# Kernel tuning notes

Hardware: AMD Instinct MI355X
Metric: run time of the kernel (lower is better)

## Reference

```python
import jax, jax.numpy as jnp
import numpy as np

B, S, I, H, F1, C = 1024, 512, 50, 64, 32, 2


def setup_inputs() -> dict:
    key = jax.random.key(0)
    ks = jax.random.split(key, 9)
    s_ih = 1.0 / np.sqrt(H)
    return {
        "x": jax.random.normal(ks[0], (B, S, I), dtype=jnp.float32),
        # PyTorch LSTM params, gate order (i, f, g, o) stacked along dim 0
        "W_ih": jax.random.uniform(ks[1], (4 * H, I), jnp.float32, -s_ih, s_ih),
        "W_hh": jax.random.uniform(ks[2], (4 * H, H), jnp.float32, -s_ih, s_ih),
        "b_ih": jax.random.uniform(ks[3], (4 * H,), jnp.float32, -s_ih, s_ih),
        "b_hh": jax.random.uniform(ks[4], (4 * H,), jnp.float32, -s_ih, s_ih),
        "W1": jax.random.uniform(ks[5], (F1, H), jnp.float32, -s_ih, s_ih),
        "b1": jax.random.uniform(ks[6], (F1,), jnp.float32, -s_ih, s_ih),
        "W2": jax.random.uniform(ks[7], (C, F1), jnp.float32, -1.0 / np.sqrt(F1), 1.0 / np.sqrt(F1)),
        "b2": jax.random.uniform(ks[8], (C,), jnp.float32, -1.0 / np.sqrt(F1), 1.0 / np.sqrt(F1)),
    }


def _lstm_last(x, W_ih, W_hh, b_ih, b_hh):
    # Precompute input contribution for all timesteps in one big GEMM: [B,S,4H]
    xg = jnp.einsum("bsi,gi->bsg", x, W_ih) + b_ih + b_hh
    Bn = x.shape[0]
    Hn = W_hh.shape[1]
    h0 = jnp.zeros((Bn, Hn), dtype=x.dtype)
    c0 = jnp.zeros((Bn, Hn), dtype=x.dtype)

    def step(carry, xt):
        h, c = carry
        g = xt + h @ W_hh.T  # [B,4H]
        i_g, f_g, g_g, o_g = jnp.split(g, 4, axis=-1)
        i_g = jax.nn.sigmoid(i_g)
        f_g = jax.nn.sigmoid(f_g)
        g_g = jnp.tanh(g_g)
        o_g = jax.nn.sigmoid(o_g)
        c_new = f_g * c + i_g * g_g
        h_new = o_g * jnp.tanh(c_new)
        return (h_new, c_new), None

    (h_last, _), _ = jax.lax.scan(step, (h0, c0), xg.transpose(1, 0, 2))
    return h_last  # == out[:, -1, :]


def reference(x, W_ih, W_hh, b_ih, b_hh, W1, b1, W2, b2):
    last_out = _lstm_last(x, W_ih, W_hh, b_ih, b_hh)
    # Dropout is identity in eval mode (deterministic reference)
    h = jax.nn.relu(last_out @ W1.T + b1)
    return h @ W2.T + b2  # [B, num_classes]
```

## Files before the change

### kernel.cpp

```cpp
#include <hip/hip_runtime.h>
#include <math.h>


#define S_LEN  512
#define I_DIM  50
#define H_DIM  64
#define BB     4
#define TC     16
#define NCH    (S_LEN / TC)
#define KROW   40
#define XROW   72
#define XSHALF (BB * TC * XROW)
#define NXE    (BB * TC * I_DIM)
#define F1_DIM 32
#define C_DIM  2
#define ILO    (1.0f / 2048.0f)

typedef __attribute__((ext_vector_type(8))) _Float16 f16x8;
typedef __attribute__((ext_vector_type(4))) float    f32x4;

__device__ __forceinline__ float fast_rcp(float x) { return __builtin_amdgcn_rcpf(x); }
__device__ __forceinline__ float sigm(float v) { return fast_rcp(1.0f + __expf(-v)); }
__device__ __forceinline__ float tanh_fast(float v) {
    return 1.0f - 2.0f * fast_rcp(__expf(2.0f * v) + 1.0f);
}

__device__ __forceinline__ void load_wfrag(const float* __restrict__ Wih,
                                           const float* __restrict__ Whh,
                                           int ktg, int row, int hk,
                                           f16x8& bh, f16x8& bl) {
    #pragma unroll
    for (int j = 0; j < 8; ++j) {
        const int kk = ktg * 32 + hk * 8 + j;
        float wv;
        if (ktg < 2) wv = (kk < I_DIM) ? Wih[row * I_DIM + kk] : 0.0f;
        else         wv = Whh[row * H_DIM + (kk - 64)];
        const _Float16 h = (_Float16)wv;
        bh[j] = h;
        bl[j] = (_Float16)((wv - (float)h) * 2048.0f);
    }
}
__device__ __forceinline__ void load_wfrag_hi(const float* __restrict__ Whh,
                                              int ktg, int row, int hk, f16x8& bh) {
    #pragma unroll
    for (int j = 0; j < 8; ++j) {
        const int kk = ktg * 32 + hk * 8 + j;
        bh[j] = (_Float16)Whh[row * H_DIM + (kk - 64)];
    }
}

#define MFMA16(A, B, C) __builtin_amdgcn_mfma_f32_16x16x32_f16(A, B, C, 0, 0, 0)

#define BAR() do { asm volatile("s_waitcnt lgkmcnt(0)" ::: "memory"); \
                   __builtin_amdgcn_s_barrier(); } while (0)

__global__ __launch_bounds__(512, 1)
void lstm_mfma(const float* __restrict__ x,
               const float* __restrict__ W_ih, const float* __restrict__ W_hh,
               const float* __restrict__ b_ih, const float* __restrict__ b_hh,
               const float* __restrict__ W1,  const float* __restrict__ b1,
               const float* __restrict__ W2,  const float* __restrict__ b2,
               float* __restrict__ out)
{
    __shared__ __align__(16) _Float16 Hst[2][2][16][KROW];
    __shared__ __align__(16) _Float16 Xs[2][BB * TC][XROW];
    __shared__ __align__(16) float    XGb[2][TC][BB][H_DIM][4];
    __shared__ float f1buf[BB][F1_DIM];

    const int u  = threadIdx.x;
    const int w  = u >> 6;
    const int l  = u & 63;
    const int c  = l & 15;
    const int hk = l >> 4;
    const int b0 = blockIdx.x * BB;
    const bool is_scan = (w < 4);
    const int q  = w & 3;
    const f32x4 Z4 = {0.f, 0.f, 0.f, 0.f};

    f16x8 s00h, s01h, s10h, s11h, s20h, s21h, s30h, s31h;
    f16x8 g00h, g00l, g01h, g01l, g10h, g10l, g11h, g11l,
          g20h, g20l, g21h, g21l, g30h, g30l, g31h, g31l;
    float bs0 = 0.f, bs1 = 0.f, bs2 = 0.f, bs3 = 0.f;
    float cst = 0.0f;

    f16x8 ga0, ga1;
    f32x4 G0, H0, G1, H1, G2, H2, G3, H3;

    const float *xp0=x,*xp1=x,*xp2=x,*xp3=x,*xp4=x,*xp5=x,*xp6=x,
                *xp7=x,*xp8=x,*xp9=x,*xp10=x,*xp11=x,*xp12=x;
    int  ld0=0,ld1=0,ld2=0,ld3=0,ld4=0,ld5=0,ld6=0,ld7=0,ld8=0,ld9=0,ld10=0,ld11=0,ld12=0;
    bool v0=false,v1=false,v2=false,v3=false,v4=false,v5=false,v6=false,
         v7=false,v8=false,v9=false,v10=false,v11=false,v12=false;

    if (is_scan) {
        const int base = 16 * w + c;
        load_wfrag_hi(W_hh, 2, 0 * H_DIM + base, hk, s00h);
        load_wfrag_hi(W_hh, 3, 0 * H_DIM + base, hk, s01h);
        load_wfrag_hi(W_hh, 2, 1 * H_DIM + base, hk, s10h);
        load_wfrag_hi(W_hh, 3, 1 * H_DIM + base, hk, s11h);
        load_wfrag_hi(W_hh, 2, 2 * H_DIM + base, hk, s20h);
        load_wfrag_hi(W_hh, 3, 2 * H_DIM + base, hk, s21h);
        load_wfrag_hi(W_hh, 2, 3 * H_DIM + base, hk, s30h);
        load_wfrag_hi(W_hh, 3, 3 * H_DIM + base, hk, s31h);
    } else {
        const int base = 16 * q + c;
        load_wfrag(W_ih, W_hh, 0, 0 * H_DIM + base, hk, g00h, g00l);
        load_wfrag(W_ih, W_hh, 1, 0 * H_DIM + base, hk, g01h, g01l);
        load_wfrag(W_ih, W_hh, 0, 1 * H_DIM + base, hk, g10h, g10l);
        load_wfrag(W_ih, W_hh, 1, 1 * H_DIM + base, hk, g11h, g11l);
        load_wfrag(W_ih, W_hh, 0, 2 * H_DIM + base, hk, g20h, g20l);
        load_wfrag(W_ih, W_hh, 1, 2 * H_DIM + base, hk, g21h, g21l);
        load_wfrag(W_ih, W_hh, 0, 3 * H_DIM + base, hk, g30h, g30l);
        load_wfrag(W_ih, W_hh, 1, 3 * H_DIM + base, hk, g31h, g31l);
        bs0 = b_ih[0 * H_DIM + base] + b_hh[0 * H_DIM + base];
        bs1 = b_ih[1 * H_DIM + base] + b_hh[1 * H_DIM + base];
        bs2 = b_ih[2 * H_DIM + base] + b_hh[2 * H_DIM + base];
        bs3 = b_ih[3 * H_DIM + base] + b_hh[3 * H_DIM + base];

        const int ug = u - 256;
#define PRE(E) { const int idx = ug + (E) * 256; if (idx < NXE) { \
            const int bb_ = idx / (TC * I_DIM); \
            const int rm_ = idx - bb_ * (TC * I_DIM); \
            const int t_  = rm_ / I_DIM; \
            const int ii_ = rm_ - t_ * I_DIM; \
            xp##E = x + (size_t)(b0 + bb_) * (S_LEN * I_DIM) + t_ * I_DIM + ii_; \
            ld##E = (bb_ * TC + t_) * XROW + ii_; v##E = true; } }
        PRE(0) PRE(1) PRE(2) PRE(3) PRE(4) PRE(5) PRE(6)
        PRE(7) PRE(8) PRE(9) PRE(10) PRE(11) PRE(12)
#undef PRE
    }

    for (int i = u; i < 1280; i += 512) ((unsigned*)Hst)[i] = 0u;
    for (int i = u; i < 4608; i += 512) ((unsigned*)Xs)[i]  = 0u;
    __syncthreads();

    if (!is_scan) {
#define STG(E, CH, BUF) if (v##E) { \
        const float t_ = xp##E[(size_t)(CH) * (TC * I_DIM)]; \
        *((_Float16*)Xs + (BUF) * XSHALF + ld##E) = (_Float16)t_; }
        STG(0,0,0) STG(1,0,0) STG(2,0,0) STG(3,0,0) STG(4,0,0) STG(5,0,0)
        STG(6,0,0) STG(7,0,0) STG(8,0,0) STG(9,0,0) STG(10,0,0) STG(11,0,0) STG(12,0,0)
        STG(0,1,1) STG(1,1,1) STG(2,1,1) STG(3,1,1) STG(4,1,1) STG(5,1,1)
        STG(6,1,1) STG(7,1,1) STG(8,1,1) STG(9,1,1) STG(10,1,1) STG(11,1,1) STG(12,1,1)
#undef STG
    }
    __syncthreads();

#define GPK(DB, MT, I) { f32x4 pk; \
    pk[0] = G0[I] + fmaf(ILO, H0[I], bs0); \
    pk[1] = G1[I] + fmaf(ILO, H1[I], bs1); \
    pk[2] = G2[I] + fmaf(ILO, H2[I], bs2); \
    pk[3] = G3[I] + fmaf(ILO, H3[I], bs3); \
    *(f32x4*)&XGb[DB][4 * hk + (I)][MT][16 * q + c][0] = pk; }

#define GQ0(SB, MT) { \
    ga0 = *(const f16x8*)&Xs[SB][(MT) * 16 + c][hk * 8]; \
    ga1 = *(const f16x8*)&Xs[SB][(MT) * 16 + c][32 + hk * 8]; \
    G0 = MFMA16(ga0, g00h, Z4); G0 = MFMA16(ga1, g01h, G0); \
    H0 = MFMA16(ga0, g00l, Z4); H0 = MFMA16(ga1, g01l, H0); }
#define GQ1() { \
    G1 = MFMA16(ga0, g10h, Z4); G1 = MFMA16(ga1, g11h, G1); \
    H1 = MFMA16(ga0, g10l, Z4); H1 = MFMA16(ga1, g11l, H1); }
#define GQ2() { \
    G2 = MFMA16(ga0, g20h, Z4); G2 = MFMA16(ga1, g21h, G2); \
    H2 = MFMA16(ga0, g20l, Z4); H2 = MFMA16(ga1, g21l, H2); }
#define GQ3(DB, MT) { \
    G3 = MFMA16(ga0, g30h, Z4); G3 = MFMA16(ga1, g31h, G3); \
    H3 = MFMA16(ga0, g30l, Z4); H3 = MFMA16(ga1, g31l, H3); \
    GPK(DB, MT, 0) GPK(DB, MT, 1) GPK(DB, MT, 2) GPK(DB, MT, 3) }

    if (!is_scan) {
        GQ0(0, 0) GQ1() GQ2() GQ3(0, 0)
        GQ0(0, 1) GQ1() GQ2() GQ3(0, 1)
        GQ0(0, 2) GQ1() GQ2() GQ3(0, 2)
        GQ0(0, 3) GQ1() GQ2() GQ3(0, 3)
    }
    __syncthreads();

#define SCAN_STEP(TT, CUR) { \
    const int p = (TT) & 1; \
    const f16x8 ah0 = *(const f16x8*)&Hst[p][0][c][hk * 8]; \
    const f16x8 ah1 = *(const f16x8*)&Hst[p][1][c][hk * 8]; \
    const f32x4 xg4 = *(const f32x4*)&XGb[CUR][TT][hk][16 * w + c][0]; \
    __builtin_amdgcn_s_setprio(1); \
    f32x4 A0 = MFMA16(ah0, s00h, ((f32x4){xg4[0], 0.f, 0.f, 0.f})); \
    A0 = MFMA16(ah1, s01h, A0); \
    f32x4 A1 = MFMA16(ah0, s10h, ((f32x4){xg4[1], 0.f, 0.f, 0.f})); \
    A1 = MFMA16(ah1, s11h, A1); \
    f32x4 A2 = MFMA16(ah0, s20h, ((f32x4){xg4[2], 0.f, 0.f, 0.f})); \
    A2 = MFMA16(ah1, s21h, A2); \
    f32x4 A3 = MFMA16(ah0, s30h, ((f32x4){xg4[3], 0.f, 0.f, 0.f})); \
    A3 = MFMA16(ah1, s31h, A3); \
    __builtin_amdgcn_s_setprio(0); \
    const float gi = sigm(A0[0]), gf = sigm(A1[0]); \
    const float gg = tanh_fast(A2[0]), go = sigm(A3[0]); \
    cst = fmaf(gf, cst, gi * gg); \
    const float hv = go * tanh_fast(cst); \
    const int uo = 16 * w + c; \
    Hst[p ^ 1][uo >> 5][4 * hk][uo & 31] = (_Float16)hv; }

#define XISS(E, CH2) if (v##E) xr##E = xp##E[(size_t)(CH2) * (TC * I_DIM)];
#define XCMT(E, BUF) if (v##E) *((_Float16*)Xs + (BUF) * XSHALF + ld##E) = (_Float16)xr##E;

    for (int ch = 0; ch < NCH; ++ch) {
        const int cur = ch & 1, nx = cur ^ 1;
        const bool cmp = (ch + 1 < NCH);
        const bool stg = (ch + 2 < NCH);
        float xr0=0,xr1=0,xr2=0,xr3=0,xr4=0,xr5=0,xr6=0,
              xr7=0,xr8=0,xr9=0,xr10=0,xr11=0,xr12=0;

        #pragma unroll
        for (int tt = 0; tt < TC; ++tt) {
            if (is_scan) {
                SCAN_STEP(tt, cur)
            } else {
                if (cmp) {
                    const int mt = tt >> 2, gq = tt & 3;
                    if (gq == 0) { GQ0(nx, mt) }
                    if (gq == 1) { GQ1() }
                    if (gq == 2) { GQ2() }
                    if (gq == 3) { GQ3(nx, mt) }
                }
                if (stg) {
                    if (tt == 0) {
                        XISS(0, ch+2) XISS(1, ch+2) XISS(2, ch+2) XISS(3, ch+2)
                        XISS(4, ch+2) XISS(5, ch+2) XISS(6, ch+2) XISS(7, ch+2)
                        XISS(8, ch+2) XISS(9, ch+2) XISS(10, ch+2) XISS(11, ch+2)
                        XISS(12, ch+2)
                    }
                    if (tt == 6)  { XCMT(0, cur)  XCMT(1, cur) }
                    if (tt == 7)  { XCMT(2, cur)  XCMT(3, cur) }
                    if (tt == 8)  { XCMT(4, cur)  XCMT(5, cur) }
                    if (tt == 9)  { XCMT(6, cur)  XCMT(7, cur) }
                    if (tt == 10) { XCMT(8, cur)  XCMT(9, cur) }
                    if (tt == 11) { XCMT(10, cur) XCMT(11, cur) }
                    if (tt == 12) { XCMT(12, cur) }
                }
            }
            BAR();
        }
    }
#undef SCAN_STEP
#undef GQ0
#undef GQ1
#undef GQ2
#undef GQ3
#undef GPK
#undef XISS
#undef XCMT

    __syncthreads();

    if (u < BB * F1_DIM) {
        const int b = u >> 5, f = u & 31;
        float acc = b1[f];
        #pragma unroll
        for (int j = 0; j < H_DIM; ++j) {
            const float hj = (float)Hst[0][j >> 5][4 * b][j & 31];
            acc = fmaf(hj, W1[f * H_DIM + j], acc);
        }
        f1buf[b][f] = fmaxf(acc, 0.0f);
    }
    __syncthreads();
    if (u < BB * C_DIM) {
        const int b = u >> 1, cl = u & 1;
        float acc = b2[cl];
        #pragma unroll
        for (int f = 0; f < F1_DIM; ++f)
            acc = fmaf(f1buf[b][f], W2[cl * F1_DIM + f], acc);
        out[(size_t)(b0 + b) * C_DIM + cl] = acc;
    }
}

extern "C" void kernel_launch(void* const* d_in, const int* in_sizes, int n_in,
                              void* d_out, int out_size, void* d_ws, size_t ws_size,
                              hipStream_t stream) {
    const float* x   = (const float*)d_in[0];
    const float* Wih = (const float*)d_in[1];
    const float* Whh = (const float*)d_in[2];
    const float* bih = (const float*)d_in[3];
    const float* bhh = (const float*)d_in[4];
    const float* W1  = (const float*)d_in[5];
    const float* b1  = (const float*)d_in[6];
    const float* W2  = (const float*)d_in[7];
    const float* b2  = (const float*)d_in[8];
    float* out = (float*)d_out;

    hipLaunchKernelGGL(lstm_mfma, dim3(256), dim3(512), 0, stream,
                       x, Wih, Whh, bih, bhh, W1, b1, W2, b2, out);
}
```

Measured before the change: 190.2 us.

## Halve batch rows per block to launch twice as many blocks

Each block now handles 2 batch rows instead of 4, so the grid doubles from 256 to 512 blocks and spreads the serial LSTM scan over more compute units. The x-staging, input-gate GEMM schedule and scan gating (only half the lanes update cell state) are reworked for the smaller tile, and launch bounds are raised to allow several blocks per CU. The cost is that half of the MFMA rows in each recurrent step are wasted, and the per-block weight loads are duplicated across more blocks.

```diff
diff --git a/kernel.cpp b/kernel.cpp
--- a/kernel.cpp
+++ b/kernel.cpp
@@ -5,7 +5,7 @@
 #define S_LEN  512
 #define I_DIM  50
 #define H_DIM  64
-#define BB     4
+#define BB     2
 #define TC     16
 #define NCH    (S_LEN / TC)
 #define KROW   40
@@ -54,7 +54,7 @@
 #define BAR() do { asm volatile("s_waitcnt lgkmcnt(0)" ::: "memory"); \
                    __builtin_amdgcn_s_barrier(); } while (0)
 
-__global__ __launch_bounds__(512, 1)
+__global__ __launch_bounds__(512, 4)
 void lstm_mfma(const float* __restrict__ x,
                const float* __restrict__ W_ih, const float* __restrict__ W_hh,
                const float* __restrict__ b_ih, const float* __restrict__ b_hh,
@@ -86,11 +86,9 @@
     f16x8 ga0, ga1;
     f32x4 G0, H0, G1, H1, G2, H2, G3, H3;
 
-    const float *xp0=x,*xp1=x,*xp2=x,*xp3=x,*xp4=x,*xp5=x,*xp6=x,
-                *xp7=x,*xp8=x,*xp9=x,*xp10=x,*xp11=x,*xp12=x;
-    int  ld0=0,ld1=0,ld2=0,ld3=0,ld4=0,ld5=0,ld6=0,ld7=0,ld8=0,ld9=0,ld10=0,ld11=0,ld12=0;
-    bool v0=false,v1=false,v2=false,v3=false,v4=false,v5=false,v6=false,
-         v7=false,v8=false,v9=false,v10=false,v11=false,v12=false;
+    const float *xp0=x,*xp1=x,*xp2=x,*xp3=x,*xp4=x,*xp5=x,*xp6=x;
+    int  ld0=0,ld1=0,ld2=0,ld3=0,ld4=0,ld5=0,ld6=0;
+    bool v0=false,v1=false,v2=false,v3=false,v4=false,v5=false,v6=false;
 
     if (is_scan) {
         const int base = 16 * w + c;
@@ -126,22 +124,19 @@
             xp##E = x + (size_t)(b0 + bb_) * (S_LEN * I_DIM) + t_ * I_DIM + ii_; \
             ld##E = (bb_ * TC + t_) * XROW + ii_; v##E = true; } }
         PRE(0) PRE(1) PRE(2) PRE(3) PRE(4) PRE(5) PRE(6)
-        PRE(7) PRE(8) PRE(9) PRE(10) PRE(11) PRE(12)
 #undef PRE
     }
 
     for (int i = u; i < 1280; i += 512) ((unsigned*)Hst)[i] = 0u;
-    for (int i = u; i < 4608; i += 512) ((unsigned*)Xs)[i]  = 0u;
+    for (int i = u; i < 2304; i += 512) ((unsigned*)Xs)[i]  = 0u;
     __syncthreads();
 
     if (!is_scan) {
 #define STG(E, CH, BUF) if (v##E) { \
         const float t_ = xp##E[(size_t)(CH) * (TC * I_DIM)]; \
         *((_Float16*)Xs + (BUF) * XSHALF + ld##E) = (_Float16)t_; }
-        STG(0,0,0) STG(1,0,0) STG(2,0,0) STG(3,0,0) STG(4,0,0) STG(5,0,0)
-        STG(6,0,0) STG(7,0,0) STG(8,0,0) STG(9,0,0) STG(10,0,0) STG(11,0,0) STG(12,0,0)
-        STG(0,1,1) STG(1,1,1) STG(2,1,1) STG(3,1,1) STG(4,1,1) STG(5,1,1)
-        STG(6,1,1) STG(7,1,1) STG(8,1,1) STG(9,1,1) STG(10,1,1) STG(11,1,1) STG(12,1,1)
+        STG(0,0,0) STG(1,0,0) STG(2,0,0) STG(3,0,0) STG(4,0,0) STG(5,0,0) STG(6,0,0)
+        STG(0,1,1) STG(1,1,1) STG(2,1,1) STG(3,1,1) STG(4,1,1) STG(5,1,1) STG(6,1,1)
 #undef STG
     }
     __syncthreads();
@@ -172,8 +167,6 @@
     if (!is_scan) {
         GQ0(0, 0) GQ1() GQ2() GQ3(0, 0)
         GQ0(0, 1) GQ1() GQ2() GQ3(0, 1)
-        GQ0(0, 2) GQ1() GQ2() GQ3(0, 2)
-        GQ0(0, 3) GQ1() GQ2() GQ3(0, 3)
     }
     __syncthreads();
 
@@ -181,7 +174,8 @@
     const int p = (TT) & 1; \
     const f16x8 ah0 = *(const f16x8*)&Hst[p][0][c][hk * 8]; \
     const f16x8 ah1 = *(const f16x8*)&Hst[p][1][c][hk * 8]; \
-    const f32x4 xg4 = *(const f32x4*)&XGb[CUR][TT][hk][16 * w + c][0]; \
+    const int bq = hk & 1; \
+    const f32x4 xg4 = *(const f32x4*)&XGb[CUR][TT][bq][16 * w + c][0]; \
     __builtin_amdgcn_s_setprio(1); \
     f32x4 A0 = MFMA16(ah0, s00h, ((f32x4){xg4[0], 0.f, 0.f, 0.f})); \
     A0 = MFMA16(ah1, s01h, A0); \
@@ -192,12 +186,14 @@
     f32x4 A3 = MFMA16(ah0, s30h, ((f32x4){xg4[3], 0.f, 0.f, 0.f})); \
     A3 = MFMA16(ah1, s31h, A3); \
     __builtin_amdgcn_s_setprio(0); \
-    const float gi = sigm(A0[0]), gf = sigm(A1[0]); \
-    const float gg = tanh_fast(A2[0]), go = sigm(A3[0]); \
-    cst = fmaf(gf, cst, gi * gg); \
-    const float hv = go * tanh_fast(cst); \
-    const int uo = 16 * w + c; \
-    Hst[p ^ 1][uo >> 5][4 * hk][uo & 31] = (_Float16)hv; }
+    if (hk < 2) { \
+        const float gi = sigm(A0[0]), gf = sigm(A1[0]); \
+        const float gg = tanh_fast(A2[0]), go = sigm(A3[0]); \
+        cst = fmaf(gf, cst, gi * gg); \
+        const float hv = go * tanh_fast(cst); \
+        const int uo = 16 * w + c; \
+        Hst[p ^ 1][uo >> 5][4 * hk][uo & 31] = (_Float16)hv; \
+    } }
 
 #define XISS(E, CH2) if (v##E) xr##E = xp##E[(size_t)(CH2) * (TC * I_DIM)];
 #define XCMT(E, BUF) if (v##E) *((_Float16*)Xs + (BUF) * XSHALF + ld##E) = (_Float16)xr##E;
@@ -206,16 +202,15 @@
         const int cur = ch & 1, nx = cur ^ 1;
         const bool cmp = (ch + 1 < NCH);
         const bool stg = (ch + 2 < NCH);
-        float xr0=0,xr1=0,xr2=0,xr3=0,xr4=0,xr5=0,xr6=0,
-              xr7=0,xr8=0,xr9=0,xr10=0,xr11=0,xr12=0;
+        float xr0=0,xr1=0,xr2=0,xr3=0,xr4=0,xr5=0,xr6=0;
 
         #pragma unroll
         for (int tt = 0; tt < TC; ++tt) {
             if (is_scan) {
                 SCAN_STEP(tt, cur)
             } else {
-                if (cmp) {
-                    const int mt = tt >> 2, gq = tt & 3;
+                if (cmp && ((tt & 1) == 0)) {
+                    const int mt = tt >> 3, gq = (tt >> 1) & 3;
                     if (gq == 0) { GQ0(nx, mt) }
                     if (gq == 1) { GQ1() }
                     if (gq == 2) { GQ2() }
@@ -224,17 +219,12 @@
                 if (stg) {
                     if (tt == 0) {
                         XISS(0, ch+2) XISS(1, ch+2) XISS(2, ch+2) XISS(3, ch+2)
-                        XISS(4, ch+2) XISS(5, ch+2) XISS(6, ch+2) XISS(7, ch+2)
-                        XISS(8, ch+2) XISS(9, ch+2) XISS(10, ch+2) XISS(11, ch+2)
-                        XISS(12, ch+2)
+                        XISS(4, ch+2) XISS(5, ch+2) XISS(6, ch+2)
                     }
                     if (tt == 6)  { XCMT(0, cur)  XCMT(1, cur) }
                     if (tt == 7)  { XCMT(2, cur)  XCMT(3, cur) }
-                    if (tt == 8)  { XCMT(4, cur)  XCMT(5, cur) }
-                    if (tt == 9)  { XCMT(6, cur)  XCMT(7, cur) }
-                    if (tt == 10) { XCMT(8, cur)  XCMT(9, cur) }
-                    if (tt == 11) { XCMT(10, cur) XCMT(11, cur) }
-                    if (tt == 12) { XCMT(12, cur) }
+                    if (tt == 9)  { XCMT(4, cur)  XCMT(5, cur) }
+                    if (tt == 11) { XCMT(6, cur) }
                 }
             }
             BAR();
@@ -286,6 +276,6 @@
     const float* b2  = (const float*)d_in[8];
     float* out = (float*)d_out;
 
-    hipLaunchKernelGGL(lstm_mfma, dim3(256), dim3(512), 0, stream,
+    hipLaunchKernelGGL(lstm_mfma, dim3(1024 / BB), dim3(512), 0, stream,
                        x, Wih, Whh, bih, bhh, W1, b1, W2, b2, out);
 }
```

Measured after the change: 466.5 us. 145% more time.
